# Optimization experiments

Measured on AMD Instinct MI355X. Metric: run time of the kernel, lower is better.

Reference implementation:

```python
import jax, jax.numpy as jnp
import numpy as np

AN = 1.0      # bandwidth a_n
SIGMA = 1.0   # Gaussian kernel scale
_EPS = 1e-32


def setup_inputs() -> dict:
    key = jax.random.key(0)
    k1, k2, k3 = jax.random.split(key, 3)
    n = 8192
    log_h = jax.random.normal(k1, (n, 1), dtype=jnp.float32)
    durations = jax.random.uniform(k2, (n,), dtype=jnp.float32)
    events = jax.random.randint(k3, (n,), 0, 2, dtype=jnp.int32)
    return {"log_h": log_h, "durations": durations, "events": events}


def reference(log_h, durations, events):
    theta = log_h.reshape(-1)                         # (n,)
    n = theta.shape[0]
    # residuals e = -(theta - log(Y)); note original adds 1e-32 before log
    e = -(theta - jnp.log(durations + _EPS))          # (n,)
    perm = jnp.argsort(e)                             # sort order of e
    e_sorted = e[perm]                                # (n,) ascending
    # Original code sorts [indices, dur, ev, theta] by the indices column,
    # which reorders the side arrays by the INVERSE permutation.
    inv = jnp.argsort(perm)
    ev = events.astype(jnp.float32)[inv]              # (n,)
    th = theta[inv]                                   # (n,)

    diff = (e_sorted[:, None] - e_sorted[None, :]) / AN   # (n, n)
    # Normal(0, SIGMA) log pdf at diff
    log_pdf = -0.5 * (diff / SIGMA) ** 2 - jnp.log(SIGMA * jnp.sqrt(2.0 * jnp.pi))
    # cond_E_i = sum_j pdf_ij * ev_j / (n*an) + eps-per-element
    cond_E = jnp.sum(jnp.exp(log_pdf) * ev / (n * AN) + _EPS, axis=1)   # (n,)
    # Normal(0, SIGMA) cdf at diff
    cdf = 0.5 * (1.0 + jax.lax.erf(diff / (SIGMA * jnp.sqrt(2.0))))
    surv = jnp.sum(cdf / n, axis=1)                   # (n,)

    loss = -jnp.sum((jnp.log(cond_E) - jnp.log(surv) + th) * ev / n)
    return loss
```

## Files before the change

### kernel.cpp

```cpp
#include <hip/hip_runtime.h>
#include <math.h>
#include <stdint.h>

#define RB 256
#define JT 512
#define GM 2048
#define YS 64

#define SCALE 0.84932180028801904f
#define SQRT2PI 2.5066282746310002f
#define KFP 0.46971863934f
#define LN2 0.69314718056f

__device__ __forceinline__ uint64_t order_key(float f, int idx) {
  unsigned u = __float_as_uint(f);
  u = (u & 0x80000000u) ? ~u : (u | 0x80000000u);
  return ((uint64_t)u << 32) | (unsigned)idx;
}

__device__ __forceinline__ void grid_geom(const float* xs, int n, float* x0, float* hx) {
  float a = xs[0] - 7.0f;
  float b = xs[n - 1] + 7.0f;
  *x0 = a;
  *hx = (b - a) / (float)(GM - 1);
}

__global__ void prep_kernel(const float* __restrict__ theta,
                            const float* __restrict__ dur,
                            float* __restrict__ e, uint64_t* __restrict__ key,
                            int* __restrict__ rank, float* __restrict__ out,
                            float* __restrict__ gbuf, int n) {
  int i = blockIdx.x * blockDim.x + threadIdx.x;
  if (i < n) {
    float ei = logf(dur[i] + 1e-32f) - theta[i];
    e[i] = ei;
    key[i] = order_key(ei, i);
    rank[i] = 0;
  }
  if (i < 4 * GM) gbuf[i] = 0.0f;
  if (i == 0) out[0] = 0.0f;
}

__global__ __launch_bounds__(RB) void rank_kernel(
    const uint64_t* __restrict__ key, int* __restrict__ rank, int n) {
  __shared__ uint64_t kt[JT];
  int i = blockIdx.x * RB + threadIdx.x;
  uint64_t ki = key[i];
  int jbase = blockIdx.y * JT;
  for (int t = threadIdx.x; t < JT; t += RB) kt[t] = key[jbase + t];
  __syncthreads();
  int cnt = 0;
  #pragma unroll 8
  for (int jj = 0; jj < JT; ++jj) cnt += (kt[jj] < ki) ? 1 : 0;
  atomicAdd(&rank[i], cnt);
}

__global__ void scatter_kernel(const float* __restrict__ e,
                               const int* __restrict__ rank,
                               const int* __restrict__ ev,
                               const float* __restrict__ theta,
                               float* __restrict__ xs, float* __restrict__ evs,
                               float* __restrict__ th_s, int n) {
  int k = blockIdx.x * blockDim.x + threadIdx.x;
  if (k < n) {
    int r = rank[k];
    xs[r] = SCALE * e[k];
    evs[k] = (float)ev[r];
    th_s[k] = theta[r];
  }
}

__global__ __launch_bounds__(RB) void gt_kernel(
    const float* __restrict__ xs, const float* __restrict__ evs,
    float* __restrict__ gbuf, int n) {
  float x0, hx;
  grid_geom(xs, n, &x0, &hx);
  int m = blockIdx.x * RB + threadIdx.x;
  float xm = fmaf((float)m, hx, x0);
  const int chunk = n / YS;
  int jb = blockIdx.y * chunk;
  const float P2S = 0.39169197f;
  float a = 0.0f, b = 0.0f, f = 0.0f, d = 0.0f;
  #pragma unroll 8
  for (int jj = 0; jj < chunk; ++jj) {
    float xj = xs[jb + jj];
    float ev = evs[jb + jj];
    float dp = xm - xj;
    float g = __builtin_amdgcn_exp2f(-(dp * dp));
    float evg = ev * g;
    a += g;
    b += evg;
    d = fmaf(dp, evg, d);
    float tt = __builtin_amdgcn_rcpf(fmaf(P2S, __builtin_fabsf(dp), 1.0f));
    float poly = tt * (0.3480242f + tt * (-0.0958798f + tt * 0.7478556f));
    f += __builtin_copysignf(fmaf(-poly, g, 1.0f), dp);
  }
  atomicAdd(&gbuf[m], a);
  atomicAdd(&gbuf[GM + m], b);
  atomicAdd(&gbuf[2 * GM + m], 0.5f * (float)chunk + 0.5f * f);
  atomicAdd(&gbuf[3 * GM + m], d);
}

__global__ __launch_bounds__(RB) void final_kernel(
    const float* __restrict__ xs, const float* __restrict__ evs,
    const float* __restrict__ th_s, const float* __restrict__ gbuf,
    float* __restrict__ out, int n) {
  float x0, hx;
  grid_geom(xs, n, &x0, &hx);
  const float* A = gbuf;
  const float* B = gbuf + GM;
  const float* F = gbuf + 2 * GM;
  const float* D = gbuf + 3 * GM;
  int i = blockIdx.x * RB + threadIdx.x;

  float term = 0.0f;
  if (i < n) {
    float x = xs[i];
    double u = ((double)x - (double)x0) / (double)hx;
    int m = (int)u;
    m = min(max(m, 0), GM - 2);
    float t = (float)(u - (double)m);
    float t2 = t * t, t3 = t2 * t;
    float h00 = 2.0f * t3 - 3.0f * t2 + 1.0f;
    float h01 = 3.0f * t2 - 2.0f * t3;
    float h10 = t3 - 2.0f * t2 + t;
    float h11 = t3 - t2;
    float Fi = F[m] * h00 + F[m + 1] * h01 +
               hx * KFP * (A[m] * h10 + A[m + 1] * h11);
    float Bi = B[m] * h00 + B[m + 1] * h01 -
               2.0f * LN2 * hx * (D[m] * h10 + D[m + 1] * h11);
    const float fn = (float)n;
    float condE = fmaxf(Bi, 0.0f) * (1.0f / SQRT2PI) / fn + fn * 1e-32f;
    float surv = fmaxf(Fi, 0.25f) / fn;
    term = (__logf(condE) - __logf(surv) + th_s[i]) * evs[i];
  }

  #pragma unroll
  for (int off = 32; off > 0; off >>= 1) term += __shfl_down(term, off, 64);
  __shared__ float red[RB / 64];
  int wave = threadIdx.x >> 6, lane = threadIdx.x & 63;
  if (lane == 0) red[wave] = term;
  __syncthreads();
  if (threadIdx.x == 0) {
    float s = 0.0f;
    #pragma unroll
    for (int w = 0; w < RB / 64; ++w) s += red[w];
    atomicAdd(out, -s / (float)n);
  }
}

extern "C" void kernel_launch(void* const* d_in, const int* in_sizes, int n_in,
                              void* d_out, int out_size, void* d_ws, size_t ws_size,
                              hipStream_t stream) {
  const float* theta = (const float*)d_in[0];
  const float* dur   = (const float*)d_in[1];
  const int*   ev    = (const int*)d_in[2];
  float* out = (float*)d_out;
  const int n = in_sizes[1];

  char* ws = (char*)d_ws;
  uint64_t* key  = (uint64_t*)ws;  ws += n * sizeof(uint64_t);
  float*    xs   = (float*)ws;     ws += n * sizeof(float);
  float*    evs  = (float*)ws;     ws += n * sizeof(float);
  float*    e    = (float*)ws;     ws += n * sizeof(float);
  int*      rank = (int*)ws;       ws += n * sizeof(int);
  float*    th_s = (float*)ws;     ws += n * sizeof(float);
  float*    gbuf = (float*)ws;     ws += 4 * GM * sizeof(float);

  int nb = (n + RB - 1) / RB;
  int nbp = (max(n, 4 * GM) + RB - 1) / RB;
  prep_kernel<<<nbp, RB, 0, stream>>>(theta, dur, e, key, rank, out, gbuf, n);
  rank_kernel<<<dim3(n / RB, n / JT), RB, 0, stream>>>(key, rank, n);
  scatter_kernel<<<nb, RB, 0, stream>>>(e, rank, ev, theta, xs, evs, th_s, n);
  gt_kernel<<<dim3(GM / RB, YS), RB, 0, stream>>>(xs, evs, gbuf, n);
  final_kernel<<<nb, RB, 0, stream>>>(xs, evs, th_s, gbuf, out, n);
}
```

Before: 83.68 us.

## Fuse rank+scatter and grid+final kernels using last-block atomic counters

```diff
diff --git a/kernel.cpp b/kernel.cpp
--- a/kernel.cpp
+++ b/kernel.cpp
@@ -28,8 +28,9 @@
 __global__ void prep_kernel(const float* __restrict__ theta,
                             const float* __restrict__ dur,
                             float* __restrict__ e, uint64_t* __restrict__ key,
-                            int* __restrict__ rank, float* __restrict__ out,
-                            float* __restrict__ gbuf, int n) {
+                            int* __restrict__ rank, float* __restrict__ gbuf,
+                            unsigned* __restrict__ cnt2, unsigned* __restrict__ cnt3,
+                            int n) {
   int i = blockIdx.x * blockDim.x + threadIdx.x;
   if (i < n) {
     float ei = logf(dur[i] + 1e-32f) - theta[i];
@@ -38,13 +39,20 @@
     rank[i] = 0;
   }
   if (i < 4 * GM) gbuf[i] = 0.0f;
-  if (i == 0) out[0] = 0.0f;
+  if (i < n / RB) cnt2[i] = 0u;
+  if (i == 0) cnt3[0] = 0u;
 }
 
-__global__ __launch_bounds__(RB) void rank_kernel(
-    const uint64_t* __restrict__ key, int* __restrict__ rank, int n) {
+__global__ __launch_bounds__(RB) void rank_scatter_kernel(
+    const uint64_t* __restrict__ key, const float* __restrict__ e,
+    const int* __restrict__ ev, const float* __restrict__ theta,
+    int* __restrict__ rank, unsigned* __restrict__ cnt2,
+    float* __restrict__ xs, float* __restrict__ evs,
+    float* __restrict__ th_s, int n) {
   __shared__ uint64_t kt[JT];
-  int i = blockIdx.x * RB + threadIdx.x;
+  __shared__ int last_flag;
+  const int ich = blockIdx.x;
+  const int i = ich * RB + threadIdx.x;
   uint64_t ki = key[i];
   int jbase = blockIdx.y * JT;
   for (int t = threadIdx.x; t < JT; t += RB) kt[t] = key[jbase + t];
@@ -53,68 +61,75 @@
   #pragma unroll 8
   for (int jj = 0; jj < JT; ++jj) cnt += (kt[jj] < ki) ? 1 : 0;
   atomicAdd(&rank[i], cnt);
-}
-
-__global__ void scatter_kernel(const float* __restrict__ e,
-                               const int* __restrict__ rank,
-                               const int* __restrict__ ev,
-                               const float* __restrict__ theta,
-                               float* __restrict__ xs, float* __restrict__ evs,
-                               float* __restrict__ th_s, int n) {
-  int k = blockIdx.x * blockDim.x + threadIdx.x;
-  if (k < n) {
-    int r = rank[k];
-    xs[r] = SCALE * e[k];
-    evs[k] = (float)ev[r];
-    th_s[k] = theta[r];
+  __threadfence();
+  __syncthreads();
+  if (threadIdx.x == 0) {
+    unsigned old = atomicAdd(&cnt2[ich], 1u);
+    last_flag = (old == gridDim.y - 1) ? 1 : 0;
+  }
+  __syncthreads();
+  if (last_flag) {
+    int r = __hip_atomic_load(&rank[i], __ATOMIC_RELAXED, __HIP_MEMORY_SCOPE_AGENT);
+    xs[r] = SCALE * e[i];
+    evs[i] = (float)ev[r];
+    th_s[i] = theta[r];
   }
 }
 
-__global__ __launch_bounds__(RB) void gt_kernel(
+__global__ __launch_bounds__(RB) void gt_final_kernel(
     const float* __restrict__ xs, const float* __restrict__ evs,
-    float* __restrict__ gbuf, int n) {
+    const float* __restrict__ th_s, float* __restrict__ gbuf,
+    unsigned* __restrict__ cnt3, float* __restrict__ out, int n) {
+  __shared__ int last_flag;
   float x0, hx;
   grid_geom(xs, n, &x0, &hx);
-  int m = blockIdx.x * RB + threadIdx.x;
-  float xm = fmaf((float)m, hx, x0);
-  const int chunk = n / YS;
-  int jb = blockIdx.y * chunk;
-  const float P2S = 0.39169197f;
-  float a = 0.0f, b = 0.0f, f = 0.0f, d = 0.0f;
-  #pragma unroll 8
-  for (int jj = 0; jj < chunk; ++jj) {
-    float xj = xs[jb + jj];
-    float ev = evs[jb + jj];
-    float dp = xm - xj;
-    float g = __builtin_amdgcn_exp2f(-(dp * dp));
-    float evg = ev * g;
-    a += g;
-    b += evg;
-    d = fmaf(dp, evg, d);
-    float tt = __builtin_amdgcn_rcpf(fmaf(P2S, __builtin_fabsf(dp), 1.0f));
-    float poly = tt * (0.3480242f + tt * (-0.0958798f + tt * 0.7478556f));
-    f += __builtin_copysignf(fmaf(-poly, g, 1.0f), dp);
+  {
+    int m = blockIdx.x * RB + threadIdx.x;
+    float xm = fmaf((float)m, hx, x0);
+    const int chunk = n / YS;
+    int jb = blockIdx.y * chunk;
+    const float P2S = 0.39169197f;
+    float a = 0.0f, b = 0.0f, f = 0.0f, d = 0.0f;
+    #pragma unroll 8
+    for (int jj = 0; jj < chunk; ++jj) {
+      float xj = xs[jb + jj];
+      float ev = evs[jb + jj];
+      float dp = xm - xj;
+      float g = __builtin_amdgcn_exp2f(-(dp * dp));
+      float evg = ev * g;
+      a += g;
+      b += evg;
+      d = fmaf(dp, evg, d);
+      float tt = __builtin_amdgcn_rcpf(fmaf(P2S, __builtin_fabsf(dp), 1.0f));
+      float poly = tt * (0.3480242f + tt * (-0.0958798f + tt * 0.7478556f));
+      f += __builtin_copysignf(fmaf(-poly, g, 1.0f), dp);
+    }
+    atomicAdd(&gbuf[m], a);
+    atomicAdd(&gbuf[GM + m], b);
+    atomicAdd(&gbuf[2 * GM + m], 0.5f * (float)chunk + 0.5f * f);
+    atomicAdd(&gbuf[3 * GM + m], d);
   }
-  atomicAdd(&gbuf[m], a);
-  atomicAdd(&gbuf[GM + m], b);
-  atomicAdd(&gbuf[2 * GM + m], 0.5f * (float)chunk + 0.5f * f);
-  atomicAdd(&gbuf[3 * GM + m], d);
-}
+  __threadfence();
+  __syncthreads();
+  if (threadIdx.x == 0) {
+    unsigned old = atomicAdd(cnt3, 1u);
+    last_flag = (old == gridDim.x * gridDim.y - 1) ? 1 : 0;
+  }
+  __syncthreads();
+  if (!last_flag) return;
 
-__global__ __launch_bounds__(RB) void final_kernel(
-    const float* __restrict__ xs, const float* __restrict__ evs,
-    const float* __restrict__ th_s, const float* __restrict__ gbuf,
-    float* __restrict__ out, int n) {
-  float x0, hx;
-  grid_geom(xs, n, &x0, &hx);
-  const float* A = gbuf;
-  const float* B = gbuf + GM;
-  const float* F = gbuf + 2 * GM;
-  const float* D = gbuf + 3 * GM;
-  int i = blockIdx.x * RB + threadIdx.x;
+  __shared__ float sA[GM], sB[GM], sF[GM], sD[GM];
+  for (int m = threadIdx.x; m < GM; m += RB) {
+    sA[m] = __hip_atomic_load(&gbuf[m],          __ATOMIC_RELAXED, __HIP_MEMORY_SCOPE_AGENT);
+    sB[m] = __hip_atomic_load(&gbuf[GM + m],     __ATOMIC_RELAXED, __HIP_MEMORY_SCOPE_AGENT);
+    sF[m] = __hip_atomic_load(&gbuf[2 * GM + m], __ATOMIC_RELAXED, __HIP_MEMORY_SCOPE_AGENT);
+    sD[m] = __hip_atomic_load(&gbuf[3 * GM + m], __ATOMIC_RELAXED, __HIP_MEMORY_SCOPE_AGENT);
+  }
+  __syncthreads();
 
-  float term = 0.0f;
-  if (i < n) {
+  float acc = 0.0f;
+  const float fn = (float)n;
+  for (int i = threadIdx.x; i < n; i += RB) {
     float x = xs[i];
     double u = ((double)x - (double)x0) / (double)hx;
     int m = (int)u;
@@ -125,27 +140,26 @@
     float h01 = 3.0f * t2 - 2.0f * t3;
     float h10 = t3 - 2.0f * t2 + t;
     float h11 = t3 - t2;
-    float Fi = F[m] * h00 + F[m + 1] * h01 +
-               hx * KFP * (A[m] * h10 + A[m + 1] * h11);
-    float Bi = B[m] * h00 + B[m + 1] * h01 -
-               2.0f * LN2 * hx * (D[m] * h10 + D[m + 1] * h11);
-    const float fn = (float)n;
+    float Fi = sF[m] * h00 + sF[m + 1] * h01 +
+               hx * KFP * (sA[m] * h10 + sA[m + 1] * h11);
+    float Bi = sB[m] * h00 + sB[m + 1] * h01 -
+               2.0f * LN2 * hx * (sD[m] * h10 + sD[m + 1] * h11);
     float condE = fmaxf(Bi, 0.0f) * (1.0f / SQRT2PI) / fn + fn * 1e-32f;
     float surv = fmaxf(Fi, 0.25f) / fn;
-    term = (__logf(condE) - __logf(surv) + th_s[i]) * evs[i];
+    acc += (__logf(condE) - __logf(surv) + th_s[i]) * evs[i];
   }
 
   #pragma unroll
-  for (int off = 32; off > 0; off >>= 1) term += __shfl_down(term, off, 64);
+  for (int off = 32; off > 0; off >>= 1) acc += __shfl_down(acc, off, 64);
   __shared__ float red[RB / 64];
   int wave = threadIdx.x >> 6, lane = threadIdx.x & 63;
-  if (lane == 0) red[wave] = term;
+  if (lane == 0) red[wave] = acc;
   __syncthreads();
   if (threadIdx.x == 0) {
     float s = 0.0f;
     #pragma unroll
     for (int w = 0; w < RB / 64; ++w) s += red[w];
-    atomicAdd(out, -s / (float)n);
+    out[0] = -s / fn;
   }
 }
 
@@ -166,12 +180,13 @@
   int*      rank = (int*)ws;       ws += n * sizeof(int);
   float*    th_s = (float*)ws;     ws += n * sizeof(float);
   float*    gbuf = (float*)ws;     ws += 4 * GM * sizeof(float);
+  unsigned* cnt2 = (unsigned*)ws;  ws += (n / RB) * sizeof(unsigned);
+  unsigned* cnt3 = (unsigned*)ws;  ws += sizeof(unsigned);
 
-  int nb = (n + RB - 1) / RB;
   int nbp = (max(n, 4 * GM) + RB - 1) / RB;
-  prep_kernel<<<nbp, RB, 0, stream>>>(theta, dur, e, key, rank, out, gbuf, n);
-  rank_kernel<<<dim3(n / RB, n / JT), RB, 0, stream>>>(key, rank, n);
-  scatter_kernel<<<nb, RB, 0, stream>>>(e, rank, ev, theta, xs, evs, th_s, n);
-  gt_kernel<<<dim3(GM / RB, YS), RB, 0, stream>>>(xs, evs, gbuf, n);
-  final_kernel<<<nb, RB, 0, stream>>>(xs, evs, th_s, gbuf, out, n);
+  prep_kernel<<<nbp, RB, 0, stream>>>(theta, dur, e, key, rank, gbuf, cnt2, cnt3, n);
+  rank_scatter_kernel<<<dim3(n / RB, n / JT), RB, 0, stream>>>(
+      key, e, ev, theta, rank, cnt2, xs, evs, th_s, n);
+  gt_final_kernel<<<dim3(GM / RB, YS), RB, 0, stream>>>(
+      xs, evs, th_s, gbuf, cnt3, out, n);
 }
```

Measured after the change: 156.3 us. 86.8% more time.

## Fold prep into rank kernel and replace rank atomics with partial-count buffer

Applied to the files above, without the earlier changes.

```diff
diff --git a/kernel.cpp b/kernel.cpp
--- a/kernel.cpp
+++ b/kernel.cpp
@@ -18,6 +18,10 @@
   return ((uint64_t)u << 32) | (unsigned)idx;
 }
 
+__device__ __forceinline__ float e_of(const float* theta, const float* dur, int i) {
+  return logf(dur[i] + 1e-32f) - theta[i];
+}
+
 __device__ __forceinline__ void grid_geom(const float* xs, int n, float* x0, float* hx) {
   float a = xs[0] - 7.0f;
   float b = xs[n - 1] + 7.0f;
@@ -25,49 +29,39 @@
   *hx = (b - a) / (float)(GM - 1);
 }
 
-__global__ void prep_kernel(const float* __restrict__ theta,
-                            const float* __restrict__ dur,
-                            float* __restrict__ e, uint64_t* __restrict__ key,
-                            int* __restrict__ rank, float* __restrict__ out,
-                            float* __restrict__ gbuf, int n) {
-  int i = blockIdx.x * blockDim.x + threadIdx.x;
-  if (i < n) {
-    float ei = logf(dur[i] + 1e-32f) - theta[i];
-    e[i] = ei;
-    key[i] = order_key(ei, i);
-    rank[i] = 0;
+__global__ __launch_bounds__(RB) void rank_part_kernel(
+    const float* __restrict__ theta, const float* __restrict__ dur,
+    int* __restrict__ rank_part, int n) {
+  __shared__ uint64_t kt[JT];
+  const int i = blockIdx.x * RB + threadIdx.x;
+  uint64_t ki = order_key(e_of(theta, dur, i), i);
+  const int jbase = blockIdx.y * JT;
+  for (int t = threadIdx.x; t < JT; t += RB) {
+    int j = jbase + t;
+    kt[t] = order_key(e_of(theta, dur, j), j);
   }
-  if (i < 4 * GM) gbuf[i] = 0.0f;
-  if (i == 0) out[0] = 0.0f;
-}
-
-__global__ __launch_bounds__(RB) void rank_kernel(
-    const uint64_t* __restrict__ key, int* __restrict__ rank, int n) {
-  __shared__ uint64_t kt[JT];
-  int i = blockIdx.x * RB + threadIdx.x;
-  uint64_t ki = key[i];
-  int jbase = blockIdx.y * JT;
-  for (int t = threadIdx.x; t < JT; t += RB) kt[t] = key[jbase + t];
   __syncthreads();
   int cnt = 0;
   #pragma unroll 8
   for (int jj = 0; jj < JT; ++jj) cnt += (kt[jj] < ki) ? 1 : 0;
-  atomicAdd(&rank[i], cnt);
+  rank_part[blockIdx.y * n + i] = cnt;
 }
 
-__global__ void scatter_kernel(const float* __restrict__ e,
-                               const int* __restrict__ rank,
-                               const int* __restrict__ ev,
-                               const float* __restrict__ theta,
-                               float* __restrict__ xs, float* __restrict__ evs,
-                               float* __restrict__ th_s, int n) {
-  int k = blockIdx.x * blockDim.x + threadIdx.x;
-  if (k < n) {
-    int r = rank[k];
-    xs[r] = SCALE * e[k];
-    evs[k] = (float)ev[r];
-    th_s[k] = theta[r];
-  }
+__global__ __launch_bounds__(RB) void scatter_kernel(
+    const float* __restrict__ theta, const float* __restrict__ dur,
+    const int* __restrict__ ev, const int* __restrict__ rank_part,
+    float* __restrict__ xs, float* __restrict__ evs, float* __restrict__ th_s,
+    float* __restrict__ gbuf, float* __restrict__ out, int n) {
+  int k = blockIdx.x * RB + threadIdx.x;
+  int r = 0;
+  const int nj = n / JT;
+  #pragma unroll 16
+  for (int jch = 0; jch < nj; ++jch) r += rank_part[jch * n + k];
+  xs[r] = SCALE * e_of(theta, dur, k);
+  evs[k] = (float)ev[r];
+  th_s[k] = theta[r];
+  if (k < 4 * GM) gbuf[k] = 0.0f;
+  if (k == 0) out[0] = 0.0f;
 }
 
 __global__ __launch_bounds__(RB) void gt_kernel(
@@ -159,19 +153,15 @@
   const int n = in_sizes[1];
 
   char* ws = (char*)d_ws;
-  uint64_t* key  = (uint64_t*)ws;  ws += n * sizeof(uint64_t);
-  float*    xs   = (float*)ws;     ws += n * sizeof(float);
-  float*    evs  = (float*)ws;     ws += n * sizeof(float);
-  float*    e    = (float*)ws;     ws += n * sizeof(float);
-  int*      rank = (int*)ws;       ws += n * sizeof(int);
-  float*    th_s = (float*)ws;     ws += n * sizeof(float);
-  float*    gbuf = (float*)ws;     ws += 4 * GM * sizeof(float);
+  int*   rank_part = (int*)ws;   ws += (n / JT) * n * sizeof(int);
+  float* xs   = (float*)ws;      ws += n * sizeof(float);
+  float* evs  = (float*)ws;      ws += n * sizeof(float);
+  float* th_s = (float*)ws;      ws += n * sizeof(float);
+  float* gbuf = (float*)ws;      ws += 4 * GM * sizeof(float);
 
-  int nb = (n + RB - 1) / RB;
-  int nbp = (max(n, 4 * GM) + RB - 1) / RB;
-  prep_kernel<<<nbp, RB, 0, stream>>>(theta, dur, e, key, rank, out, gbuf, n);
-  rank_kernel<<<dim3(n / RB, n / JT), RB, 0, stream>>>(key, rank, n);
-  scatter_kernel<<<nb, RB, 0, stream>>>(e, rank, ev, theta, xs, evs, th_s, n);
+  rank_part_kernel<<<dim3(n / RB, n / JT), RB, 0, stream>>>(theta, dur, rank_part, n);
+  scatter_kernel<<<n / RB, RB, 0, stream>>>(theta, dur, ev, rank_part,
+                                            xs, evs, th_s, gbuf, out, n);
   gt_kernel<<<dim3(GM / RB, YS), RB, 0, stream>>>(xs, evs, gbuf, n);
-  final_kernel<<<nb, RB, 0, stream>>>(xs, evs, th_s, gbuf, out, n);
+  final_kernel<<<n / RB, RB, 0, stream>>>(xs, evs, th_s, gbuf, out, n);
 }
```

Result: faster. 81.53 us (-2.6%).
